# Optimization experiments

Hardware: AMD Instinct MI355X
Metric: run time of the kernel (lower is better)

The kernel has to match this reference:

```python
import jax, jax.numpy as jnp
import numpy as np

D_MODEL = 768
NUM_HEADS = 12
D_K = D_MODEL // NUM_HEADS
B, T = 2, 4096


def setup_inputs() -> dict:
    key = jax.random.key(0)
    ks = jax.random.split(key, 5)
    x = jax.random.normal(ks[0], (B, T, D_MODEL), dtype=jnp.float32)
    # causal mask: True = masked (matches masked_fill semantics)
    mask = jnp.triu(jnp.ones((T, T), dtype=bool), k=1)
    W_qkv = jax.random.normal(ks[1], (D_MODEL, 3 * D_MODEL), dtype=jnp.float32) / np.sqrt(D_MODEL)
    b_qkv = jax.random.normal(ks[2], (3 * D_MODEL,), dtype=jnp.float32) * 0.02
    W_out = jax.random.normal(ks[3], (D_MODEL, D_MODEL), dtype=jnp.float32) / np.sqrt(D_MODEL)
    b_out = jax.random.normal(ks[4], (D_MODEL,), dtype=jnp.float32) * 0.02
    return {"x": x, "mask": mask, "W_qkv": W_qkv, "b_qkv": b_qkv, "W_out": W_out, "b_out": b_out}


def reference(x, mask, W_qkv, b_qkv, W_out, b_out):
    Bb, Tt, C = x.shape
    qkv = x @ W_qkv + b_qkv                       # [B,T,3C]
    # torch: reshape(B,T,H,3*d_k).transpose(1,2) then chunk on last dim
    qkv = qkv.reshape(Bb, Tt, NUM_HEADS, 3, D_K)  # split each head's 3*d_k chunk
    qkv = jnp.transpose(qkv, (0, 2, 1, 3, 4))     # [B,H,T,3,d_k]
    q, k, v = qkv[..., 0, :], qkv[..., 1, :], qkv[..., 2, :]
    scores = jnp.einsum('bhqd,bhkd->bhqk', q, k) / np.sqrt(D_K)
    scores = jnp.where(mask[None, None], -jnp.inf, scores)
    attn = jax.nn.softmax(scores, axis=-1)
    context = jnp.einsum('bhqk,bhkd->bhqd', attn, v)
    context = jnp.transpose(context, (0, 2, 1, 3)).reshape(Bb, Tt, C)
    return context @ W_out + b_out
```

## Files before the change

kernel.cpp:

```cpp
#include <hip/hip_runtime.h>
#include <hip/hip_bf16.h>
#include <stdint.h>


typedef __attribute__((ext_vector_type(8))) short bf16x8;
typedef __attribute__((ext_vector_type(4))) short bf16x4;
typedef __attribute__((ext_vector_type(4))) float f32x4;

#define TT 4096
#define NH 12
#define DK 64
#define DMODEL 768
#define NQKV 2304

__device__ __forceinline__ unsigned short f2bf(float f) {
    union { float f; unsigned u; } v; v.f = f;
    unsigned u = v.u;
    return (unsigned short)((u + 0x7fffu + ((u >> 16) & 1u)) >> 16);
}
__device__ __forceinline__ unsigned fbits(float f) {
    union { float f; unsigned u; } v; v.f = f; return v.u;
}
__device__ __forceinline__ unsigned pack_bf2(float a, float b) {
    return __builtin_amdgcn_perm(fbits(b) + 0x8000u, fbits(a) + 0x8000u, 0x07060302u);
}
__device__ __forceinline__ void glds16(const void* g, void* l) {
    __builtin_amdgcn_global_load_lds(
        (const __attribute__((address_space(1))) void*)g,
        (__attribute__((address_space(3))) void*)l, 16, 0, 0);
}

__global__ __launch_bounds__(256)
void prep(const float* __restrict__ x, unsigned short* __restrict__ xb,
          const float* __restrict__ Wq, unsigned short* __restrict__ Wqt,
          const float* __restrict__ Wo, unsigned short* __restrict__ Wot) {
    int b = blockIdx.x;
    if (b < 6144) {
        int i = (b * 256 + threadIdx.x) * 4;
        float4 v = *(const float4*)(x + i);
        uint2 u;
        u.x = pack_bf2(v.x, v.y);
        u.y = pack_bf2(v.z, v.w);
        *(uint2*)(xb + i) = u;
        return;
    }
    __shared__ unsigned short tile[64][65];
    const float* W; unsigned short* Wt; int K, N, bx, by;
    if (b < 6144 + 432) {
        int bb = b - 6144; bx = bb % 36; by = bb / 36;
        W = Wq; Wt = Wqt; K = DMODEL; N = NQKV;
    } else {
        int bb = b - 6576; bx = bb % 12; by = bb / 12;
        W = Wo; Wt = Wot; K = DMODEL; N = DMODEL;
    }
    int k0 = by * 64, n0 = bx * 64;
    int c = threadIdx.x & 63;
    int r0 = threadIdx.x >> 6;
    for (int p = 0; p < 16; ++p) {
        int r = r0 + p * 4;
        tile[r][c] = f2bf(W[(size_t)(k0 + r) * N + n0 + c]);
    }
    __syncthreads();
    for (int p = 0; p < 16; ++p) {
        int n = r0 + p * 4;
        Wt[(size_t)(n0 + n) * K + k0 + c] = tile[c][n];
    }
}

__global__ __launch_bounds__(256, 3)
void gemm_qkv(const unsigned short* __restrict__ Amat, const unsigned short* __restrict__ Bmat,
              const float* __restrict__ bias, unsigned short* __restrict__ qb,
              unsigned short* __restrict__ kb, unsigned short* __restrict__ vtb) {
    __shared__ unsigned short As[128 * 64];
    __shared__ unsigned short Bs[128 * 64];
    const int K = DMODEL;
    int m0 = blockIdx.y * 128, n0 = blockIdx.x * 128;
    int tid = threadIdx.x, lane = tid & 63, w = tid >> 6;
    int wm = (w >> 1) * 64, wn = (w & 1) * 64;
    int quad = lane >> 4, lc = lane & 15;

    const unsigned short* agp[4]; const unsigned short* bgp[4];
    unsigned short* alp[4]; unsigned short* blp[4];
    for (int p = 0; p < 4; ++p) {
        int c = (w * 4 + p) * 64 + lane;
        int row = c >> 3, pc = c & 7;
        int gc = pc ^ (row & 7);
        agp[p] = Amat + (size_t)(m0 + row) * K + gc * 8;
        bgp[p] = Bmat + (size_t)(n0 + row) * K + gc * 8;
        alp[p] = &As[(w * 4 + p) * 512];
        blp[p] = &Bs[(w * 4 + p) * 512];
    }
    int foff[4][2];
    for (int mt = 0; mt < 4; ++mt)
        for (int h = 0; h < 2; ++h)
            foff[mt][h] = (mt * 16 + lc) * 64 + (((quad + 4 * h) ^ (lc & 7)) * 8);

    f32x4 acc[4][4];
    for (int a = 0; a < 4; ++a)
        for (int b2 = 0; b2 < 4; ++b2) acc[a][b2] = (f32x4){0.f, 0.f, 0.f, 0.f};

    for (int k0 = 0; k0 < K; k0 += 64) {
        for (int p = 0; p < 4; ++p) {
            glds16(agp[p] + k0, alp[p]);
            glds16(bgp[p] + k0, blp[p]);
        }
        __syncthreads();
        bf16x8 af[4][2], bfr[4][2];
        for (int mt = 0; mt < 4; ++mt)
            for (int h = 0; h < 2; ++h) {
                af[mt][h]  = *(const bf16x8*)(&As[wm * 64 + foff[mt][h]]);
                bfr[mt][h] = *(const bf16x8*)(&Bs[wn * 64 + foff[mt][h]]);
            }
        for (int mt = 0; mt < 4; ++mt)
            for (int nt = 0; nt < 4; ++nt) {
                acc[mt][nt] = __builtin_amdgcn_mfma_f32_16x16x32_bf16(
                    af[mt][0], bfr[nt][0], acc[mt][nt], 0, 0, 0);
                acc[mt][nt] = __builtin_amdgcn_mfma_f32_16x16x32_bf16(
                    af[mt][1], bfr[nt][1], acc[mt][nt], 0, 0, 0);
            }
        __syncthreads();
    }
    const float c2q = 0.18033688f;
    for (int mt = 0; mt < 4; ++mt) {
        int colv = m0 + wm + mt * 16 + quad * 4;
        float4 bv = *(const float4*)(bias + colv);
        int h = colv / 192;
        int r = colv - h * 192;
        int which = r >> 6;
        int d0 = r & 63;
        for (int nt = 0; nt < 4; ++nt) {
            int tok = n0 + wn + nt * 16 + lc;
            int b = tok >> 12, t = tok & 4095;
            size_t bh = (size_t)(b * NH + h);
            float v0 = acc[mt][nt][0] + bv.x, v1 = acc[mt][nt][1] + bv.y;
            float v2 = acc[mt][nt][2] + bv.z, v3 = acc[mt][nt][3] + bv.w;
            if (which == 0) {
                uint2 u;
                u.x = pack_bf2(v0 * c2q, v1 * c2q);
                u.y = pack_bf2(v2 * c2q, v3 * c2q);
                *(uint2*)(qb + (bh * TT + t) * DK + d0) = u;
            } else if (which == 1) {
                uint2 u;
                u.x = pack_bf2(v0, v1);
                u.y = pack_bf2(v2, v3);
                *(uint2*)(kb + (bh * TT + t) * DK + d0) = u;
            } else {
                unsigned short* vp = vtb + (bh * DK + d0) * TT + t;
                vp[0] = f2bf(v0); vp[TT] = f2bf(v1);
                vp[2 * TT] = f2bf(v2); vp[3 * TT] = f2bf(v3);
            }
        }
    }
}

template <bool DIAG>
__device__ __forceinline__ void flash_tile(const unsigned short* __restrict__ Kb,
                                           const unsigned short* __restrict__ Vb,
                                           bf16x8 qf0, bf16x8 qf1,
                                           f32x4 (&o)[4], f32x4& ol,
                                           int kt, int q_lo, int quad, int lc) {
    int c0 = quad ^ (lc & 7);
    int sw = lc & 7;
    const bf16x4 ones = {(short)0x3F80, (short)0x3F80, (short)0x3F80, (short)0x3F80};
    for (int ktile = 0; ktile < 4; ++ktile) {
        bf16x8 kf0 = *(const bf16x8*)(&Kb[(ktile * 16 + lc) * 64 + c0 * 8]);
        bf16x8 kf1 = *(const bf16x8*)(&Kb[(ktile * 16 + lc) * 64 + (c0 ^ 4) * 8]);
        f32x4 s = (f32x4){0.f, 0.f, 0.f, 0.f};
        s = __builtin_amdgcn_mfma_f32_16x16x32_bf16(kf0, qf0, s, 0, 0, 0);
        s = __builtin_amdgcn_mfma_f32_16x16x32_bf16(kf1, qf1, s, 0, 0, 0);
        float p[4];
        if (DIAG) {
            int key0 = kt + ktile * 16 + quad * 4;
            int qcol = q_lo + lc;
            for (int i = 0; i < 4; ++i) {
                float e = __builtin_amdgcn_exp2f(s[i]);
                if (key0 + i > qcol) e = 0.f;
                p[i] = e;
            }
        } else {
            for (int i = 0; i < 4; ++i) p[i] = __builtin_amdgcn_exp2f(s[i]);
        }
        union { uint2 u; bf16x4 v; } pc;
        pc.u.x = pack_bf2(p[0], p[1]);
        pc.u.y = pack_bf2(p[2], p[3]);
        ol = __builtin_amdgcn_mfma_f32_16x16x16bf16_1k(ones, pc.v, ol, 0, 0, 0);
        int c8 = (ktile * 2 + (quad >> 1)) ^ sw;
        int voff = c8 * 8 + (quad & 1) * 4;
        for (int dt = 0; dt < 4; ++dt) {
            bf16x4 vf = *(const bf16x4*)(&Vb[(dt * 16 + lc) * 64 + voff]);
            o[dt] = __builtin_amdgcn_mfma_f32_16x16x16bf16_1k(vf, pc.v, o[dt], 0, 0, 0);
        }
    }
}

__global__ __launch_bounds__(256)
void flash_attn(const unsigned short* __restrict__ qbuf,
                const unsigned short* __restrict__ kbuf,
                const unsigned short* __restrict__ vtbuf,
                unsigned short* __restrict__ ctx) {
    __shared__ unsigned short Ks[2][64 * 64];
    __shared__ unsigned short Vs[2][64 * 64];
    int bh = blockIdx.x;
    int qblk = 63 - (int)blockIdx.y;
    int tid = threadIdx.x, lane = tid & 63, w = tid >> 6;
    int quad = lane >> 4, lc = lane & 15;
    const size_t base = (size_t)bh * TT * DK;
    const unsigned short* kb = kbuf + base;
    const unsigned short* vb = vtbuf + base;
    int col8 = ((lane & 7) ^ (lane >> 3)) * 8;
    int klane = (lane >> 3) * DK + col8;
    int vlane = (lane >> 3) * TT + col8;
    size_t hb = (size_t)(bh / NH) * TT * DMODEL + (size_t)(bh % NH) * DK;

    int q_lo = qblk * 64 + w * 16;
    int ntile = qblk + 1;

    bf16x8 qf0, qf1;
    {
        const unsigned short* qp = qbuf + base + (size_t)(q_lo + lc) * DK;
        qf0 = *(const bf16x8*)(qp + quad * 8);
        qf1 = *(const bf16x8*)(qp + 32 + quad * 8);
    }
    f32x4 o[4];
    for (int dt = 0; dt < 4; ++dt) o[dt] = (f32x4){0.f, 0.f, 0.f, 0.f};
    f32x4 ol = (f32x4){0.f, 0.f, 0.f, 0.f};

    {
        int rb = (w & 1) * 4;
        if (w < 2)
            for (int r = 0; r < 4; ++r)
                glds16(kb + (size_t)((rb + r) * 8) * DK + klane, &Ks[0][(rb + r) * 512]);
        else
            for (int r = 0; r < 4; ++r)
                glds16(vb + (size_t)((rb + r) * 8) * TT + vlane, &Vs[0][(rb + r) * 512]);
    }
    __syncthreads();

    for (int ti = 0; ti < ntile; ++ti) {
        int cur = ti & 1;
        if (ti + 1 < ntile) {
            int kn = (ti + 1) * 64;
            int rb = (w & 1) * 4;
            if (w < 2)
                for (int r = 0; r < 4; ++r)
                    glds16(kb + (size_t)(kn + (rb + r) * 8) * DK + klane,
                           &Ks[cur ^ 1][(rb + r) * 512]);
            else
                for (int r = 0; r < 4; ++r)
                    glds16(vb + (size_t)((rb + r) * 8) * TT + kn + vlane,
                           &Vs[cur ^ 1][(rb + r) * 512]);
        }
        int kt = ti * 64;
        if (ti == ntile - 1)
            flash_tile<true>(&Ks[cur][0], &Vs[cur][0], qf0, qf1, o, ol,
                             kt, q_lo, quad, lc);
        else
            flash_tile<false>(&Ks[cur][0], &Vs[cur][0], qf0, qf1, o, ol,
                              kt, q_lo, quad, lc);
        __syncthreads();
    }

    float inv = 1.f / ol[0];
    int t = q_lo + lc;
    unsigned short* cp = ctx + hb + (size_t)t * DMODEL;
    for (int dt = 0; dt < 4; ++dt) {
        uint2 u;
        u.x = pack_bf2(o[dt][0] * inv, o[dt][1] * inv);
        u.y = pack_bf2(o[dt][2] * inv, o[dt][3] * inv);
        *(uint2*)(cp + dt * 16 + quad * 4) = u;
    }
}

__global__ __launch_bounds__(256, 4)
void gemm_out(const unsigned short* __restrict__ Amat, const unsigned short* __restrict__ Bmat,
              const float* __restrict__ bias, float* __restrict__ out) {
    __shared__ unsigned short S[(64 + 128) * 64];
    const int K = DMODEL;
    int m0 = blockIdx.y * 64, n0 = blockIdx.x * 128;
    int tid = threadIdx.x, lane = tid & 63, w = tid >> 6;
    int wm = (w & 1) * 32, wn = (w >> 1) * 64;
    int quad = lane >> 4, lc = lane & 15;

    const unsigned short* gp[6]; unsigned short* lp[6];
    for (int p = 0; p < 6; ++p) {
        int c = (w * 6 + p) * 64 + lane;
        if (c < 512) {
            int row = c >> 3, gc = (c & 7) ^ (row & 7);
            gp[p] = Amat + (size_t)(m0 + row) * K + gc * 8;
        } else {
            int cb = c - 512;
            int row = cb >> 3, gc = (cb & 7) ^ (row & 7);
            gp[p] = Bmat + (size_t)(n0 + row) * K + gc * 8;
        }
        lp[p] = &S[(w * 6 + p) * 512];
    }
    int foffA[2][2], foffB[4][2];
    for (int mt = 0; mt < 2; ++mt)
        for (int h = 0; h < 2; ++h)
            foffA[mt][h] = (wm + mt * 16 + lc) * 64 + (((quad + 4 * h) ^ (lc & 7)) * 8);
    for (int nt = 0; nt < 4; ++nt)
        for (int h = 0; h < 2; ++h)
            foffB[nt][h] = 4096 + (wn + nt * 16 + lc) * 64 + (((quad + 4 * h) ^ (lc & 7)) * 8);

    f32x4 acc[2][4];
    for (int a = 0; a < 2; ++a)
        for (int b2 = 0; b2 < 4; ++b2) acc[a][b2] = (f32x4){0.f, 0.f, 0.f, 0.f};

    for (int k0 = 0; k0 < K; k0 += 64) {
        for (int p = 0; p < 6; ++p) glds16(gp[p] + k0, lp[p]);
        __syncthreads();
        bf16x8 af[2][2], bfr[4][2];
        for (int mt = 0; mt < 2; ++mt)
            for (int h = 0; h < 2; ++h) af[mt][h] = *(const bf16x8*)(&S[foffA[mt][h]]);
        for (int nt = 0; nt < 4; ++nt)
            for (int h = 0; h < 2; ++h) bfr[nt][h] = *(const bf16x8*)(&S[foffB[nt][h]]);
        for (int mt = 0; mt < 2; ++mt)
            for (int nt = 0; nt < 4; ++nt) {
                acc[mt][nt] = __builtin_amdgcn_mfma_f32_16x16x32_bf16(
                    af[mt][0], bfr[nt][0], acc[mt][nt], 0, 0, 0);
                acc[mt][nt] = __builtin_amdgcn_mfma_f32_16x16x32_bf16(
                    af[mt][1], bfr[nt][1], acc[mt][nt], 0, 0, 0);
            }
        __syncthreads();
    }
    for (int mt = 0; mt < 2; ++mt) {
        int colv = m0 + wm + mt * 16 + quad * 4;
        float4 bv = *(const float4*)(bias + colv);
        for (int nt = 0; nt < 4; ++nt) {
            int tok = n0 + wn + nt * 16 + lc;
            float4 ov;
            ov.x = acc[mt][nt][0] + bv.x;
            ov.y = acc[mt][nt][1] + bv.y;
            ov.z = acc[mt][nt][2] + bv.z;
            ov.w = acc[mt][nt][3] + bv.w;
            *(float4*)(out + (size_t)tok * DMODEL + colv) = ov;
        }
    }
}

extern "C" void kernel_launch(void* const* d_in, const int* in_sizes, int n_in,
                              void* d_out, int out_size, void* d_ws, size_t ws_size,
                              hipStream_t stream) {
    const float* x     = (const float*)d_in[0];
    const float* W_qkv = (const float*)d_in[2];
    const float* b_qkv = (const float*)d_in[3];
    const float* W_out = (const float*)d_in[4];
    const float* b_out = (const float*)d_in[5];
    float* out = (float*)d_out;

    unsigned short* ws = (unsigned short*)d_ws;
    unsigned short* Wqkv_t = ws;
    unsigned short* Wout_t = Wqkv_t + (size_t)NQKV * DMODEL;
    unsigned short* q_buf  = Wout_t + (size_t)DMODEL * DMODEL;
    unsigned short* k_buf  = q_buf  + (size_t)2 * NH * TT * DK;
    unsigned short* vt_buf = k_buf  + (size_t)2 * NH * TT * DK;
    unsigned short* ctx    = vt_buf + (size_t)2 * NH * TT * DK;
    unsigned short* x_bf   = ctx;

    prep<<<dim3(6720), 256, 0, stream>>>(x, x_bf, W_qkv, Wqkv_t, W_out, Wout_t);
    gemm_qkv<<<dim3((2 * TT) / 128, NQKV / 128), 256, 0, stream>>>(
        Wqkv_t, x_bf, b_qkv, q_buf, k_buf, vt_buf);
    flash_attn<<<dim3(2 * NH, TT / 64), 256, 0, stream>>>(q_buf, k_buf, vt_buf, ctx);
    gemm_out<<<dim3((2 * TT) / 128, DMODEL / 64), 256, 0, stream>>>(
        Wout_t, ctx, b_out, out);
}
```

Baseline: 262.3 us.

## Process two query fragments per wave to reuse K/V LDS reads in flash attention

```diff
diff --git a/kernel.cpp b/kernel.cpp
--- a/kernel.cpp
+++ b/kernel.cpp
@@ -156,44 +156,49 @@
 template <bool DIAG>
 __device__ __forceinline__ void flash_tile(const unsigned short* __restrict__ Kb,
                                            const unsigned short* __restrict__ Vb,
-                                           bf16x8 qf0, bf16x8 qf1,
-                                           f32x4 (&o)[4], f32x4& ol,
-                                           int kt, int q_lo, int quad, int lc) {
+                                           const bf16x8 (&qf)[2][2],
+                                           f32x4 (&o)[2][4], f32x4 (&ol)[2],
+                                           int kt, int q0, int quad, int lc) {
     int c0 = quad ^ (lc & 7);
     int sw = lc & 7;
     const bf16x4 ones = {(short)0x3F80, (short)0x3F80, (short)0x3F80, (short)0x3F80};
     for (int ktile = 0; ktile < 4; ++ktile) {
         bf16x8 kf0 = *(const bf16x8*)(&Kb[(ktile * 16 + lc) * 64 + c0 * 8]);
         bf16x8 kf1 = *(const bf16x8*)(&Kb[(ktile * 16 + lc) * 64 + (c0 ^ 4) * 8]);
-        f32x4 s = (f32x4){0.f, 0.f, 0.f, 0.f};
-        s = __builtin_amdgcn_mfma_f32_16x16x32_bf16(kf0, qf0, s, 0, 0, 0);
-        s = __builtin_amdgcn_mfma_f32_16x16x32_bf16(kf1, qf1, s, 0, 0, 0);
-        float p[4];
-        if (DIAG) {
-            int key0 = kt + ktile * 16 + quad * 4;
-            int qcol = q_lo + lc;
-            for (int i = 0; i < 4; ++i) {
-                float e = __builtin_amdgcn_exp2f(s[i]);
-                if (key0 + i > qcol) e = 0.f;
-                p[i] = e;
-            }
-        } else {
-            for (int i = 0; i < 4; ++i) p[i] = __builtin_amdgcn_exp2f(s[i]);
-        }
-        union { uint2 u; bf16x4 v; } pc;
-        pc.u.x = pack_bf2(p[0], p[1]);
-        pc.u.y = pack_bf2(p[2], p[3]);
-        ol = __builtin_amdgcn_mfma_f32_16x16x16bf16_1k(ones, pc.v, ol, 0, 0, 0);
+        bf16x4 pcv[2];
+        for (int f = 0; f < 2; ++f) {
+            f32x4 s = (f32x4){0.f, 0.f, 0.f, 0.f};
+            s = __builtin_amdgcn_mfma_f32_16x16x32_bf16(kf0, qf[f][0], s, 0, 0, 0);
+            s = __builtin_amdgcn_mfma_f32_16x16x32_bf16(kf1, qf[f][1], s, 0, 0, 0);
+            float p[4];
+            if (DIAG) {
+                int key0 = kt + ktile * 16 + quad * 4;
+                int qcol = q0 + f * 16 + lc;
+                for (int i = 0; i < 4; ++i) {
+                    float e = __builtin_amdgcn_exp2f(s[i]);
+                    if (key0 + i > qcol) e = 0.f;
+                    p[i] = e;
+                }
+            } else {
+                for (int i = 0; i < 4; ++i) p[i] = __builtin_amdgcn_exp2f(s[i]);
+            }
+            union { uint2 u; bf16x4 v; } pc;
+            pc.u.x = pack_bf2(p[0], p[1]);
+            pc.u.y = pack_bf2(p[2], p[3]);
+            pcv[f] = pc.v;
+            ol[f] = __builtin_amdgcn_mfma_f32_16x16x16bf16_1k(ones, pcv[f], ol[f], 0, 0, 0);
+        }
         int c8 = (ktile * 2 + (quad >> 1)) ^ sw;
         int voff = c8 * 8 + (quad & 1) * 4;
         for (int dt = 0; dt < 4; ++dt) {
             bf16x4 vf = *(const bf16x4*)(&Vb[(dt * 16 + lc) * 64 + voff]);
-            o[dt] = __builtin_amdgcn_mfma_f32_16x16x16bf16_1k(vf, pc.v, o[dt], 0, 0, 0);
-        }
-    }
-}
-
-__global__ __launch_bounds__(256)
+            o[0][dt] = __builtin_amdgcn_mfma_f32_16x16x16bf16_1k(vf, pcv[0], o[0][dt], 0, 0, 0);
+            o[1][dt] = __builtin_amdgcn_mfma_f32_16x16x16bf16_1k(vf, pcv[1], o[1][dt], 0, 0, 0);
+        }
+    }
+}
+
+__global__ __launch_bounds__(128)
 void flash_attn(const unsigned short* __restrict__ qbuf,
                 const unsigned short* __restrict__ kbuf,
                 const unsigned short* __restrict__ vtbuf,
@@ -212,27 +217,29 @@
     int vlane = (lane >> 3) * TT + col8;
     size_t hb = (size_t)(bh / NH) * TT * DMODEL + (size_t)(bh % NH) * DK;
 
-    int q_lo = qblk * 64 + w * 16;
+    int q0 = qblk * 64 + w * 32;
     int ntile = qblk + 1;
 
-    bf16x8 qf0, qf1;
+    bf16x8 qf[2][2];
+    for (int f = 0; f < 2; ++f) {
+        const unsigned short* qp = qbuf + base + (size_t)(q0 + f * 16 + lc) * DK;
+        qf[f][0] = *(const bf16x8*)(qp + quad * 8);
+        qf[f][1] = *(const bf16x8*)(qp + 32 + quad * 8);
+    }
+    f32x4 o[2][4];
+    for (int f = 0; f < 2; ++f)
+        for (int dt = 0; dt < 4; ++dt) o[f][dt] = (f32x4){0.f, 0.f, 0.f, 0.f};
+    f32x4 ol[2];
+    ol[0] = (f32x4){0.f, 0.f, 0.f, 0.f};
+    ol[1] = (f32x4){0.f, 0.f, 0.f, 0.f};
+
     {
-        const unsigned short* qp = qbuf + base + (size_t)(q_lo + lc) * DK;
-        qf0 = *(const bf16x8*)(qp + quad * 8);
-        qf1 = *(const bf16x8*)(qp + 32 + quad * 8);
-    }
-    f32x4 o[4];
-    for (int dt = 0; dt < 4; ++dt) o[dt] = (f32x4){0.f, 0.f, 0.f, 0.f};
-    f32x4 ol = (f32x4){0.f, 0.f, 0.f, 0.f};
-
-    {
-        int rb = (w & 1) * 4;
-        if (w < 2)
-            for (int r = 0; r < 4; ++r)
-                glds16(kb + (size_t)((rb + r) * 8) * DK + klane, &Ks[0][(rb + r) * 512]);
+        if (w == 0)
+            for (int r = 0; r < 8; ++r)
+                glds16(kb + (size_t)(r * 8) * DK + klane, &Ks[0][r * 512]);
         else
-            for (int r = 0; r < 4; ++r)
-                glds16(vb + (size_t)((rb + r) * 8) * TT + vlane, &Vs[0][(rb + r) * 512]);
+            for (int r = 0; r < 8; ++r)
+                glds16(vb + (size_t)(r * 8) * TT + vlane, &Vs[0][r * 512]);
     }
     __syncthreads();
 
@@ -240,34 +247,35 @@
         int cur = ti & 1;
         if (ti + 1 < ntile) {
             int kn = (ti + 1) * 64;
-            int rb = (w & 1) * 4;
-            if (w < 2)
-                for (int r = 0; r < 4; ++r)
-                    glds16(kb + (size_t)(kn + (rb + r) * 8) * DK + klane,
-                           &Ks[cur ^ 1][(rb + r) * 512]);
+            if (w == 0)
+                for (int r = 0; r < 8; ++r)
+                    glds16(kb + (size_t)(kn + r * 8) * DK + klane,
+                           &Ks[cur ^ 1][r * 512]);
             else
-                for (int r = 0; r < 4; ++r)
-                    glds16(vb + (size_t)((rb + r) * 8) * TT + kn + vlane,
-                           &Vs[cur ^ 1][(rb + r) * 512]);
+                for (int r = 0; r < 8; ++r)
+                    glds16(vb + (size_t)(r * 8) * TT + kn + vlane,
+                           &Vs[cur ^ 1][r * 512]);
         }
         int kt = ti * 64;
         if (ti == ntile - 1)
-            flash_tile<true>(&Ks[cur][0], &Vs[cur][0], qf0, qf1, o, ol,
-                             kt, q_lo, quad, lc);
+            flash_tile<true>(&Ks[cur][0], &Vs[cur][0], qf, o, ol,
+                             kt, q0, quad, lc);
         else
-            flash_tile<false>(&Ks[cur][0], &Vs[cur][0], qf0, qf1, o, ol,
-                              kt, q_lo, quad, lc);
-        __syncthreads();
-    }
-
-    float inv = 1.f / ol[0];
-    int t = q_lo + lc;
-    unsigned short* cp = ctx + hb + (size_t)t * DMODEL;
-    for (int dt = 0; dt < 4; ++dt) {
-        uint2 u;
-        u.x = pack_bf2(o[dt][0] * inv, o[dt][1] * inv);
-        u.y = pack_bf2(o[dt][2] * inv, o[dt][3] * inv);
-        *(uint2*)(cp + dt * 16 + quad * 4) = u;
+            flash_tile<false>(&Ks[cur][0], &Vs[cur][0], qf, o, ol,
+                              kt, q0, quad, lc);
+        __syncthreads();
+    }
+
+    for (int f = 0; f < 2; ++f) {
+        float inv = 1.f / ol[f][0];
+        int t = q0 + f * 16 + lc;
+        unsigned short* cp = ctx + hb + (size_t)t * DMODEL;
+        for (int dt = 0; dt < 4; ++dt) {
+            uint2 u;
+            u.x = pack_bf2(o[f][dt][0] * inv, o[f][dt][1] * inv);
+            u.y = pack_bf2(o[f][dt][2] * inv, o[f][dt][3] * inv);
+            *(uint2*)(cp + dt * 16 + quad * 4) = u;
+        }
     }
 }
 
@@ -360,7 +368,7 @@
     prep<<<dim3(6720), 256, 0, stream>>>(x, x_bf, W_qkv, Wqkv_t, W_out, Wout_t);
     gemm_qkv<<<dim3((2 * TT) / 128, NQKV / 128), 256, 0, stream>>>(
         Wqkv_t, x_bf, b_qkv, q_buf, k_buf, vt_buf);
-    flash_attn<<<dim3(2 * NH, TT / 64), 256, 0, stream>>>(q_buf, k_buf, vt_buf, ctx);
+    flash_attn<<<dim3(2 * NH, TT / 64), 128, 0, stream>>>(q_buf, k_buf, vt_buf, ctx);
     gemm_out<<<dim3((2 * TT) / 128, DMODEL / 64), 256, 0, stream>>>(
         Wout_t, ctx, b_out, out);
 }
```

New measurement: 280.2 us. +6.9%, slower.

## Split flash-attention key tile across warps and reduce partial outputs through LDS

Applied to the files above, without the earlier changes.

```diff
diff --git a/kernel.cpp b/kernel.cpp
--- a/kernel.cpp
+++ b/kernel.cpp
@@ -156,22 +156,23 @@
 template <bool DIAG>
 __device__ __forceinline__ void flash_tile(const unsigned short* __restrict__ Kb,
                                            const unsigned short* __restrict__ Vb,
-                                           bf16x8 qf0, bf16x8 qf1,
-                                           f32x4 (&o)[4], f32x4& ol,
-                                           int kt, int q_lo, int quad, int lc) {
+                                           const bf16x8 (&qf)[4][2],
+                                           f32x4 (&o)[4][4], f32x4 (&ol)[4],
+                                           int kt, int q0, int w, int quad, int lc) {
     int c0 = quad ^ (lc & 7);
     int sw = lc & 7;
     const bf16x4 ones = {(short)0x3F80, (short)0x3F80, (short)0x3F80, (short)0x3F80};
-    for (int ktile = 0; ktile < 4; ++ktile) {
-        bf16x8 kf0 = *(const bf16x8*)(&Kb[(ktile * 16 + lc) * 64 + c0 * 8]);
-        bf16x8 kf1 = *(const bf16x8*)(&Kb[(ktile * 16 + lc) * 64 + (c0 ^ 4) * 8]);
+    bf16x8 kf0 = *(const bf16x8*)(&Kb[(w * 16 + lc) * 64 + c0 * 8]);
+    bf16x8 kf1 = *(const bf16x8*)(&Kb[(w * 16 + lc) * 64 + (c0 ^ 4) * 8]);
+    bf16x4 pcv[4];
+    for (int qt = 0; qt < 4; ++qt) {
         f32x4 s = (f32x4){0.f, 0.f, 0.f, 0.f};
-        s = __builtin_amdgcn_mfma_f32_16x16x32_bf16(kf0, qf0, s, 0, 0, 0);
-        s = __builtin_amdgcn_mfma_f32_16x16x32_bf16(kf1, qf1, s, 0, 0, 0);
+        s = __builtin_amdgcn_mfma_f32_16x16x32_bf16(kf0, qf[qt][0], s, 0, 0, 0);
+        s = __builtin_amdgcn_mfma_f32_16x16x32_bf16(kf1, qf[qt][1], s, 0, 0, 0);
         float p[4];
         if (DIAG) {
-            int key0 = kt + ktile * 16 + quad * 4;
-            int qcol = q_lo + lc;
+            int key0 = kt + w * 16 + quad * 4;
+            int qcol = q0 + qt * 16 + lc;
             for (int i = 0; i < 4; ++i) {
                 float e = __builtin_amdgcn_exp2f(s[i]);
                 if (key0 + i > qcol) e = 0.f;
@@ -183,13 +184,15 @@
         union { uint2 u; bf16x4 v; } pc;
         pc.u.x = pack_bf2(p[0], p[1]);
         pc.u.y = pack_bf2(p[2], p[3]);
-        ol = __builtin_amdgcn_mfma_f32_16x16x16bf16_1k(ones, pc.v, ol, 0, 0, 0);
-        int c8 = (ktile * 2 + (quad >> 1)) ^ sw;
-        int voff = c8 * 8 + (quad & 1) * 4;
-        for (int dt = 0; dt < 4; ++dt) {
-            bf16x4 vf = *(const bf16x4*)(&Vb[(dt * 16 + lc) * 64 + voff]);
-            o[dt] = __builtin_amdgcn_mfma_f32_16x16x16bf16_1k(vf, pc.v, o[dt], 0, 0, 0);
-        }
+        pcv[qt] = pc.v;
+        ol[qt] = __builtin_amdgcn_mfma_f32_16x16x16bf16_1k(ones, pcv[qt], ol[qt], 0, 0, 0);
+    }
+    int c8 = (w * 2 + (quad >> 1)) ^ sw;
+    int voff = c8 * 8 + (quad & 1) * 4;
+    for (int dt = 0; dt < 4; ++dt) {
+        bf16x4 vf = *(const bf16x4*)(&Vb[(dt * 16 + lc) * 64 + voff]);
+        for (int qt = 0; qt < 4; ++qt)
+            o[qt][dt] = __builtin_amdgcn_mfma_f32_16x16x16bf16_1k(vf, pcv[qt], o[qt][dt], 0, 0, 0);
     }
 }
 
@@ -198,8 +201,10 @@
                 const unsigned short* __restrict__ kbuf,
                 const unsigned short* __restrict__ vtbuf,
                 unsigned short* __restrict__ ctx) {
-    __shared__ unsigned short Ks[2][64 * 64];
-    __shared__ unsigned short Vs[2][64 * 64];
+    __shared__ __align__(16) unsigned char smem[32768];
+    float* o_acc = (float*)smem;
+    float* l_acc = (float*)(smem + 17408);
+
     int bh = blockIdx.x;
     int qblk = 63 - (int)blockIdx.y;
     int tid = threadIdx.x, lane = tid & 63, w = tid >> 6;
@@ -212,27 +217,31 @@
     int vlane = (lane >> 3) * TT + col8;
     size_t hb = (size_t)(bh / NH) * TT * DMODEL + (size_t)(bh % NH) * DK;
 
-    int q_lo = qblk * 64 + w * 16;
+    int q0 = qblk * 64;
     int ntile = qblk + 1;
 
-    bf16x8 qf0, qf1;
-    {
-        const unsigned short* qp = qbuf + base + (size_t)(q_lo + lc) * DK;
-        qf0 = *(const bf16x8*)(qp + quad * 8);
-        qf1 = *(const bf16x8*)(qp + 32 + quad * 8);
-    }
-    f32x4 o[4];
-    for (int dt = 0; dt < 4; ++dt) o[dt] = (f32x4){0.f, 0.f, 0.f, 0.f};
-    f32x4 ol = (f32x4){0.f, 0.f, 0.f, 0.f};
+    bf16x8 qf[4][2];
+    for (int qt = 0; qt < 4; ++qt) {
+        const unsigned short* qp = qbuf + base + (size_t)(q0 + qt * 16 + lc) * DK;
+        qf[qt][0] = *(const bf16x8*)(qp + quad * 8);
+        qf[qt][1] = *(const bf16x8*)(qp + 32 + quad * 8);
+    }
+    f32x4 o[4][4];
+    for (int qt = 0; qt < 4; ++qt)
+        for (int dt = 0; dt < 4; ++dt) o[qt][dt] = (f32x4){0.f, 0.f, 0.f, 0.f};
+    f32x4 ol[4];
+    for (int qt = 0; qt < 4; ++qt) ol[qt] = (f32x4){0.f, 0.f, 0.f, 0.f};
 
     {
         int rb = (w & 1) * 4;
         if (w < 2)
             for (int r = 0; r < 4; ++r)
-                glds16(kb + (size_t)((rb + r) * 8) * DK + klane, &Ks[0][(rb + r) * 512]);
+                glds16(kb + (size_t)((rb + r) * 8) * DK + klane,
+                       (unsigned short*)(smem) + (rb + r) * 512);
         else
             for (int r = 0; r < 4; ++r)
-                glds16(vb + (size_t)((rb + r) * 8) * TT + vlane, &Vs[0][(rb + r) * 512]);
+                glds16(vb + (size_t)((rb + r) * 8) * TT + vlane,
+                       (unsigned short*)(smem + 16384) + (rb + r) * 512);
     }
     __syncthreads();
 
@@ -241,33 +250,60 @@
         if (ti + 1 < ntile) {
             int kn = (ti + 1) * 64;
             int rb = (w & 1) * 4;
+            unsigned short* Kalt = (unsigned short*)(smem + (cur ^ 1) * 8192);
+            unsigned short* Valt = (unsigned short*)(smem + 16384 + (cur ^ 1) * 8192);
             if (w < 2)
                 for (int r = 0; r < 4; ++r)
                     glds16(kb + (size_t)(kn + (rb + r) * 8) * DK + klane,
-                           &Ks[cur ^ 1][(rb + r) * 512]);
+                           Kalt + (rb + r) * 512);
             else
                 for (int r = 0; r < 4; ++r)
                     glds16(vb + (size_t)((rb + r) * 8) * TT + kn + vlane,
-                           &Vs[cur ^ 1][(rb + r) * 512]);
+                           Valt + (rb + r) * 512);
         }
         int kt = ti * 64;
+        const unsigned short* Kcur = (const unsigned short*)(smem + cur * 8192);
+        const unsigned short* Vcur = (const unsigned short*)(smem + 16384 + cur * 8192);
         if (ti == ntile - 1)
-            flash_tile<true>(&Ks[cur][0], &Vs[cur][0], qf0, qf1, o, ol,
-                             kt, q_lo, quad, lc);
+            flash_tile<true>(Kcur, Vcur, qf, o, ol, kt, q0, w, quad, lc);
         else
-            flash_tile<false>(&Ks[cur][0], &Vs[cur][0], qf0, qf1, o, ol,
-                              kt, q_lo, quad, lc);
-        __syncthreads();
-    }
-
-    float inv = 1.f / ol[0];
-    int t = q_lo + lc;
-    unsigned short* cp = ctx + hb + (size_t)t * DMODEL;
-    for (int dt = 0; dt < 4; ++dt) {
-        uint2 u;
-        u.x = pack_bf2(o[dt][0] * inv, o[dt][1] * inv);
-        u.y = pack_bf2(o[dt][2] * inv, o[dt][3] * inv);
-        *(uint2*)(cp + dt * 16 + quad * 4) = u;
+            flash_tile<false>(Kcur, Vcur, qf, o, ol, kt, q0, w, quad, lc);
+        __syncthreads();
+    }
+
+    for (int r = 0; r < 4; ++r) {
+        if (w == r) {
+            for (int qt = 0; qt < 4; ++qt) {
+                int row = qt * 16 + lc;
+                float* bp = o_acc + row * 68 + quad * 4;
+                if (r == 0) {
+                    for (int dt = 0; dt < 4; ++dt)
+                        *(f32x4*)(bp + dt * 16) = o[qt][dt];
+                    if (quad == 0) l_acc[row] = ol[qt][0];
+                } else {
+                    for (int dt = 0; dt < 4; ++dt) {
+                        f32x4 t = *(const f32x4*)(bp + dt * 16);
+                        *(f32x4*)(bp + dt * 16) = t + o[qt][dt];
+                    }
+                    if (quad == 0) l_acc[row] += ol[qt][0];
+                }
+            }
+        }
+        __syncthreads();
+    }
+
+    {
+        int row = w * 16 + lc;
+        float inv = 1.f / l_acc[row];
+        int t = q0 + row;
+        unsigned short* cp = ctx + hb + (size_t)t * DMODEL;
+        for (int dt = 0; dt < 4; ++dt) {
+            f32x4 ov = *(const f32x4*)(o_acc + row * 68 + dt * 16 + quad * 4);
+            uint2 u;
+            u.x = pack_bf2(ov[0] * inv, ov[1] * inv);
+            u.y = pack_bf2(ov[2] * inv, ov[3] * inv);
+            *(uint2*)(cp + dt * 16 + quad * 4) = u;
+        }
     }
 }
 
```

Measured after the change: 278.9 us. +6.3%, slower.

## Use 32-key KV tiles with per-warp causal skip and balanced query-block order

Applied to the files above, without the earlier changes.

```diff
diff --git a/kernel.cpp b/kernel.cpp
--- a/kernel.cpp
+++ b/kernel.cpp
@@ -154,15 +154,15 @@
 }
 
 template <bool DIAG>
-__device__ __forceinline__ void flash_tile(const unsigned short* __restrict__ Kb,
-                                           const unsigned short* __restrict__ Vb,
-                                           bf16x8 qf0, bf16x8 qf1,
-                                           f32x4 (&o)[4], f32x4& ol,
-                                           int kt, int q_lo, int quad, int lc) {
+__device__ __forceinline__ void flash_tile32(const unsigned short* __restrict__ Kb,
+                                             const unsigned short* __restrict__ Vb,
+                                             bf16x8 qf0, bf16x8 qf1,
+                                             f32x4 (&o)[4], f32x4& ol,
+                                             int kt, int q_lo, int quad, int lc) {
     int c0 = quad ^ (lc & 7);
-    int sw = lc & 7;
+    int fv = (lc >> 1) & 3;
     const bf16x4 ones = {(short)0x3F80, (short)0x3F80, (short)0x3F80, (short)0x3F80};
-    for (int ktile = 0; ktile < 4; ++ktile) {
+    for (int ktile = 0; ktile < 2; ++ktile) {
         bf16x8 kf0 = *(const bf16x8*)(&Kb[(ktile * 16 + lc) * 64 + c0 * 8]);
         bf16x8 kf1 = *(const bf16x8*)(&Kb[(ktile * 16 + lc) * 64 + (c0 ^ 4) * 8]);
         f32x4 s = (f32x4){0.f, 0.f, 0.f, 0.f};
@@ -184,24 +184,25 @@
         pc.u.x = pack_bf2(p[0], p[1]);
         pc.u.y = pack_bf2(p[2], p[3]);
         ol = __builtin_amdgcn_mfma_f32_16x16x16bf16_1k(ones, pc.v, ol, 0, 0, 0);
-        int c8 = (ktile * 2 + (quad >> 1)) ^ sw;
-        int voff = c8 * 8 + (quad & 1) * 4;
+        int c_swz = (ktile * 2 + (quad >> 1)) ^ fv;
+        int voff = c_swz * 8 + (quad & 1) * 4;
         for (int dt = 0; dt < 4; ++dt) {
-            bf16x4 vf = *(const bf16x4*)(&Vb[(dt * 16 + lc) * 64 + voff]);
+            bf16x4 vf = *(const bf16x4*)(&Vb[(dt * 16 + lc) * 32 + voff]);
             o[dt] = __builtin_amdgcn_mfma_f32_16x16x16bf16_1k(vf, pc.v, o[dt], 0, 0, 0);
         }
     }
 }
 
-__global__ __launch_bounds__(256)
+__global__ __launch_bounds__(256, 8)
 void flash_attn(const unsigned short* __restrict__ qbuf,
                 const unsigned short* __restrict__ kbuf,
                 const unsigned short* __restrict__ vtbuf,
                 unsigned short* __restrict__ ctx) {
-    __shared__ unsigned short Ks[2][64 * 64];
-    __shared__ unsigned short Vs[2][64 * 64];
+    __shared__ __align__(16) unsigned char smem[16384];
+
     int bh = blockIdx.x;
-    int qblk = 63 - (int)blockIdx.y;
+    int yy = (int)blockIdx.y;
+    int qblk = (yy & 1) ? (yy >> 1) : (63 - (yy >> 1));
     int tid = threadIdx.x, lane = tid & 63, w = tid >> 6;
     int quad = lane >> 4, lc = lane & 15;
     const size_t base = (size_t)bh * TT * DK;
@@ -209,11 +210,12 @@
     const unsigned short* vb = vtbuf + base;
     int col8 = ((lane & 7) ^ (lane >> 3)) * 8;
     int klane = (lane >> 3) * DK + col8;
-    int vlane = (lane >> 3) * TT + col8;
+    int vrow = lane >> 2;
+    int vchunk = ((lane & 3) ^ ((lane >> 3) & 3)) * 8;
     size_t hb = (size_t)(bh / NH) * TT * DMODEL + (size_t)(bh % NH) * DK;
 
     int q_lo = qblk * 64 + w * 16;
-    int ntile = qblk + 1;
+    int ntile = 2 * qblk + 2;
 
     bf16x8 qf0, qf1;
     {
@@ -226,37 +228,49 @@
     f32x4 ol = (f32x4){0.f, 0.f, 0.f, 0.f};
 
     {
-        int rb = (w & 1) * 4;
-        if (w < 2)
-            for (int r = 0; r < 4; ++r)
-                glds16(kb + (size_t)((rb + r) * 8) * DK + klane, &Ks[0][(rb + r) * 512]);
-        else
-            for (int r = 0; r < 4; ++r)
-                glds16(vb + (size_t)((rb + r) * 8) * TT + vlane, &Vs[0][(rb + r) * 512]);
+        if (w < 2) {
+            for (int r = 0; r < 2; ++r) {
+                int g = w * 2 + r;
+                glds16(kb + (size_t)(g * 8) * DK + klane,
+                       (unsigned short*)smem + g * 512);
+            }
+        } else {
+            for (int r = 0; r < 2; ++r) {
+                int g = (w - 2) * 2 + r;
+                glds16(vb + (size_t)(g * 16 + vrow) * TT + vchunk,
+                       (unsigned short*)(smem + 8192) + g * 512);
+            }
+        }
     }
     __syncthreads();
 
     for (int ti = 0; ti < ntile; ++ti) {
         int cur = ti & 1;
         if (ti + 1 < ntile) {
-            int kn = (ti + 1) * 64;
-            int rb = (w & 1) * 4;
-            if (w < 2)
-                for (int r = 0; r < 4; ++r)
-                    glds16(kb + (size_t)(kn + (rb + r) * 8) * DK + klane,
-                           &Ks[cur ^ 1][(rb + r) * 512]);
+            int kn = (ti + 1) * 32;
+            if (w < 2) {
+                unsigned short* Kalt = (unsigned short*)(smem + (cur ^ 1) * 4096);
+                for (int r = 0; r < 2; ++r) {
+                    int g = w * 2 + r;
+                    glds16(kb + (size_t)(kn + g * 8) * DK + klane, Kalt + g * 512);
+                }
+            } else {
+                unsigned short* Valt = (unsigned short*)(smem + 8192 + (cur ^ 1) * 4096);
+                for (int r = 0; r < 2; ++r) {
+                    int g = (w - 2) * 2 + r;
+                    glds16(vb + (size_t)(g * 16 + vrow) * TT + kn + vchunk, Valt + g * 512);
+                }
+            }
+        }
+        int kt = ti * 32;
+        if (kt <= q_lo + 15) {
+            const unsigned short* Kcur = (const unsigned short*)(smem + cur * 4096);
+            const unsigned short* Vcur = (const unsigned short*)(smem + 8192 + cur * 4096);
+            if (kt + 31 > q_lo)
+                flash_tile32<true>(Kcur, Vcur, qf0, qf1, o, ol, kt, q_lo, quad, lc);
             else
-                for (int r = 0; r < 4; ++r)
-                    glds16(vb + (size_t)((rb + r) * 8) * TT + kn + vlane,
-                           &Vs[cur ^ 1][(rb + r) * 512]);
-        }
-        int kt = ti * 64;
-        if (ti == ntile - 1)
-            flash_tile<true>(&Ks[cur][0], &Vs[cur][0], qf0, qf1, o, ol,
-                             kt, q_lo, quad, lc);
-        else
-            flash_tile<false>(&Ks[cur][0], &Vs[cur][0], qf0, qf1, o, ol,
-                              kt, q_lo, quad, lc);
+                flash_tile32<false>(Kcur, Vcur, qf0, qf1, o, ol, kt, q_lo, quad, lc);
+        }
         __syncthreads();
     }
 
```

Result: slower. 275.6 us (+5.1%).
